# Kernel optimization log

Hardware: AMD Instinct MI355X
Metric: run time of the kernel (lower is better)

The kernel has to match this reference:

```python
import jax, jax.numpy as jnp
import numpy as np
from jax import lax

B, CHI, CHO, H, W = 8, 128, 128, 64, 64
K = 3
KK = K * K


def setup_inputs() -> dict:
    key = jax.random.key(0)
    ks = jax.random.split(key, 7)
    x = jax.random.normal(ks[0], (B, CHI, H, W), jnp.float32)
    # small offset-conv weights so sampled offsets stay in a realistic few-pixel range
    off_w = jax.random.normal(ks[1], (3 * KK, CHI, K, K), jnp.float32) * 0.01
    off_b = jnp.zeros((3 * KK,), jnp.float32)
    w = jax.random.normal(ks[2], (CHO, CHI, K, K), jnp.float32) / np.sqrt(CHI * KK).astype(np.float32)
    b = jnp.zeros((CHO,), jnp.float32)
    gamma = jax.random.uniform(ks[3], (CHO,), jnp.float32)  # nn.init.uniform_ on BN weight
    beta = jnp.zeros((CHO,), jnp.float32)
    return {"x": x, "off_w": off_w, "off_b": off_b, "w": w, "b": b, "gamma": gamma, "beta": beta}


def _deform_conv(x, off_w, off_b, w, b):
    """DCNv2 modulated deformable conv, k=3, stride=1, pad=1, dil=1, 1 deform group."""
    B_, C, H_, W_ = x.shape
    # offset/mask branch: plain 3x3 conv -> 27 channels (2*9 offsets, 9 masks)
    om = lax.conv_general_dilated(x, off_w, (1, 1), ((1, 1), (1, 1)),
                                  dimension_numbers=("NCHW", "OIHW", "NCHW"))
    om = om + off_b[None, :, None, None]
    off = om[:, : 2 * KK].reshape(B_, KK, 2, H_, W_)  # [B,9,2,H,W]; ch 2k=y, 2k+1=x
    mask = jax.nn.sigmoid(om[:, 2 * KK:])             # [B,9,H,W]

    ky, kx = jnp.meshgrid(jnp.arange(K, dtype=jnp.float32),
                          jnp.arange(K, dtype=jnp.float32), indexing="ij")
    ky = ky.reshape(KK); kx = kx.reshape(KK)
    # sampling positions: p = p0 - pad + k*dil + offset
    py = off[:, :, 0] + (jnp.arange(H_, dtype=jnp.float32) - 1.0)[None, None, :, None] + ky[None, :, None, None]
    px = off[:, :, 1] + (jnp.arange(W_, dtype=jnp.float32) - 1.0)[None, None, None, :] + kx[None, :, None, None]

    y0 = jnp.floor(py); x0 = jnp.floor(px)
    ly = py - y0; lx = px - x0
    xf = x.reshape(B_, C, H_ * W_)

    def corner(yi, xi, wgt):
        valid = ((yi >= 0) & (yi <= H_ - 1) & (xi >= 0) & (xi <= W_ - 1)).astype(x.dtype)
        yc = jnp.clip(yi, 0, H_ - 1).astype(jnp.int32)
        xc = jnp.clip(xi, 0, W_ - 1).astype(jnp.int32)
        idx = (yc * W_ + xc).reshape(B_, KK * H_ * W_)
        g = jax.vmap(lambda xb, ib: xb[:, ib])(xf, idx).reshape(B_, C, KK, H_, W_)
        return g * (valid * wgt)[:, None]

    val = (corner(y0, x0, (1 - ly) * (1 - lx))
           + corner(y0, x0 + 1, (1 - ly) * lx)
           + corner(y0 + 1, x0, ly * (1 - lx))
           + corner(y0 + 1, x0 + 1, ly * lx))  # [B,C,9,H,W]
    val = val * mask[:, None]  # modulation
    out = jnp.einsum("bckhw,ock->bohw", val, w.reshape(w.shape[0], C, KK))
    return out + b[None, :, None, None]


def reference(x, off_w, off_b, w, b, gamma, beta):
    y = _deform_conv(x, off_w, off_b, w, b)
    # BatchNorm2d in training mode (batch statistics), eps=1e-5, then ReLU
    mean = y.mean(axis=(0, 2, 3))
    var = y.var(axis=(0, 2, 3))
    yn = (y - mean[None, :, None, None]) * lax.rsqrt(var[None, :, None, None] + 1e-5)
    return jax.nn.relu(yn * gamma[None, :, None, None] + beta[None, :, None, None])
```

## Files before the change

kernel.cpp:

```cpp
#include <hip/hip_runtime.h>
#include <hip/hip_bf16.h>
#include <math.h>

#define HH 64
#define WW 64
#define HW 4096
#define LDV 136

typedef __bf16 bf16x8 __attribute__((ext_vector_type(8)));
typedef float floatx4 __attribute__((ext_vector_type(4)));
typedef unsigned int uint4a __attribute__((ext_vector_type(4)));
typedef unsigned int uint2a __attribute__((ext_vector_type(2)));

#define WS_Y    0u
#define WS_PSQ  16777216u
#define WS_XTB  16778240u
#define WS_WTB  25166848u
#define WS_OWB  25461760u

static __device__ inline ushort f2bf(float f) {
  __hip_bfloat16 h = __float2bfloat16(f);
  return __builtin_bit_cast(ushort, h);
}
static __device__ inline float lo16(unsigned int u) { return __builtin_bit_cast(float, u << 16); }
static __device__ inline float hi16(unsigned int u) { return __builtin_bit_cast(float, u & 0xffff0000u); }

__global__ __launch_bounds__(256) void k_prep(const float* __restrict__ x,
                                              const float* __restrict__ w,
                                              const float* __restrict__ ow,
                                              ushort* __restrict__ xtb,
                                              ushort* __restrict__ wtb,
                                              ushort* __restrict__ owb,
                                              float* __restrict__ psq) {
  __shared__ float tile[32][33];
  int bid = blockIdx.x;
  if (bid < 4096) {
    int hw0 = (bid & 127) * 32;
    int c0 = ((bid >> 7) & 3) * 32;
    int b = bid >> 9;
    int col = threadIdx.x & 31, row = threadIdx.x >> 5;
    const float* xb = x + ((size_t)b * 128 + c0) * HW + hw0;
#pragma unroll
    for (int i = 0; i < 32; i += 8)
      tile[row + i][col] = xb[(size_t)(row + i) * HW + col];
    __syncthreads();
    int hw = threadIdx.x >> 3, cq = threadIdx.x & 7;
    ushort* xo = xtb + ((size_t)b * HW + hw0) * 128 + c0;
    unsigned int lo = (unsigned int)f2bf(tile[cq * 4 + 0][hw]) |
                      ((unsigned int)f2bf(tile[cq * 4 + 1][hw]) << 16);
    unsigned int hi = (unsigned int)f2bf(tile[cq * 4 + 2][hw]) |
                      ((unsigned int)f2bf(tile[cq * 4 + 3][hw]) << 16);
    uint2a v2 = (uint2a){lo, hi};
    *(uint2a*)(&xo[(size_t)hw * 128 + cq * 4]) = v2;
  } else if (bid < 4096 + 576) {
    int idx = (bid - 4096) * 256 + threadIdx.x;
    int c = idx & 127, o = (idx >> 7) & 127, k = idx >> 14;
    wtb[idx] = f2bf(w[(o * 128 + c) * 9 + k]);
  } else if (bid < 4096 + 720) {
    int j = (bid - 4672) * 256 + threadIdx.x;
    int c = j & 127, o = (j >> 7) & 31, k = j >> 12;
    float v = (o < 27) ? ow[(o * 128 + c) * 9 + k] : 0.f;
    owb[j] = f2bf(v);
  } else {
    psq[threadIdx.x] = 0.f;
  }
}

__global__ __launch_bounds__(256) void k_main(
    const ushort* __restrict__ xtb, const ushort* __restrict__ wtb,
    const ushort* __restrict__ owb, const float* __restrict__ off_b,
    const float* __restrict__ bias, float* __restrict__ y) {
  __shared__ alignas(16) ushort Vl[2][32 * LDV];
  __shared__ float omL[27 * 32];
  int t = threadIdx.x;
  int lane = t & 63, wv = t >> 6;
  int li = lane & 15, quad = lane >> 4;
  int hr = blockIdx.x;
  int row = hr >> 1, p0b = (hr & 1) * 32;
  int b = blockIdx.y;
  const ushort* xb = xtb + (size_t)b * HW * 128;
  int ch = t & 15;
  int pq = t >> 4;

  int mi = wv & 1, ni = wv >> 1;
  floatx4 oacc = (floatx4){0.f, 0.f, 0.f, 0.f};
  uint4a u0, u1;
  auto p1load = [&](int k, int p, uint4a& u) {
    int ky = k / 3, kx = k % 3;
    int ry = row - 1 + ky, cx = p0b + p - 1 + kx;
    bool v = (ry >= 0 && ry < HH && cx >= 0 && cx < WW);
    int idx = v ? (ry * WW + cx) : 0;
    uint4a a = *(const uint4a*)(xb + (size_t)idx * 128 + ch * 8);
    u = v ? a : (uint4a){0u, 0u, 0u, 0u};
  };
  p1load(0, pq, u0);
  p1load(0, pq + 16, u1);
  for (int k = 0; k < 9; ++k) {
    *(uint4a*)(&Vl[k & 1][pq * LDV + ch * 8]) = u0;
    *(uint4a*)(&Vl[k & 1][(pq + 16) * LDV + ch * 8]) = u1;
    if (k < 8) {
      p1load(k + 1, pq, u0);
      p1load(k + 1, pq + 16, u1);
    }
    __syncthreads();
#pragma unroll
    for (int ks = 0; ks < 4; ++ks) {
      bf16x8 bfrag = __builtin_bit_cast(bf16x8,
          *(const uint4a*)(&Vl[k & 1][(ni * 16 + li) * LDV + ks * 32 + quad * 8]));
      bf16x8 afrag = __builtin_bit_cast(bf16x8,
          *(const uint4a*)(&owb[(size_t)(k * 32 + mi * 16 + li) * 128 + ks * 32 + quad * 8]));
      oacc = __builtin_amdgcn_mfma_f32_16x16x32_bf16(afrag, bfrag, oacc, 0, 0, 0);
    }
  }
#pragma unroll
  for (int r = 0; r < 4; ++r) {
    int o = mi * 16 + quad * 4 + r;
    if (o < 27) omL[o * 32 + ni * 16 + li] = oacc[r] + off_b[o];
  }
  __syncthreads();

  floatx4 macc[8][2];
#pragma unroll
  for (int g = 0; g < 8; ++g) {
    macc[g][0] = (floatx4){0.f, 0.f, 0.f, 0.f};
    macc[g][1] = (floatx4){0.f, 0.f, 0.f, 0.f};
  }

  float wqA[4], wqB[4];
  int idxA[4], idxB[4];
  uint4a u[8];

  auto prep = [&](int k, int p, float* wq, int* idx4) {
    int ky = k / 3, kx = k % 3;
    float offy = omL[(2 * k) * 32 + p];
    float offx = omL[(2 * k + 1) * 32 + p];
    float mraw = omL[(18 + k) * 32 + p];
    float m = 1.f / (1.f + __expf(-mraw));
    float py = offy + (float)(row - 1 + ky);
    float px = offx + (float)(p0b + p - 1 + kx);
    float y0f = floorf(py), x0f = floorf(px);
    float ly = py - y0f, lx = px - x0f;
    int iy0 = (int)y0f, ix0 = (int)x0f;
    int iy1 = iy0 + 1, ix1 = ix0 + 1;
    float w00 = (1.f - ly) * (1.f - lx) * m, w01 = (1.f - ly) * lx * m;
    float w10 = ly * (1.f - lx) * m, w11 = ly * lx * m;
    if (iy0 < 0 || iy0 > HH - 1) { w00 = 0.f; w01 = 0.f; }
    if (iy1 < 0 || iy1 > HH - 1) { w10 = 0.f; w11 = 0.f; }
    if (ix0 < 0 || ix0 > WW - 1) { w00 = 0.f; w10 = 0.f; }
    if (ix1 < 0 || ix1 > WW - 1) { w01 = 0.f; w11 = 0.f; }
    int cy0 = min(max(iy0, 0), HH - 1), cy1 = min(max(iy1, 0), HH - 1);
    int cx0 = min(max(ix0, 0), WW - 1), cx1 = min(max(ix1, 0), WW - 1);
    idx4[0] = cy0 * WW + cx0;
    idx4[1] = cy0 * WW + cx1;
    idx4[2] = cy1 * WW + cx0;
    idx4[3] = cy1 * WW + cx1;
    wq[0] = w00; wq[1] = w01; wq[2] = w10; wq[3] = w11;
  };
  auto issue = [&]() {
#pragma unroll
    for (int c = 0; c < 4; ++c)
      u[c] = *(const uint4a*)(xb + (size_t)idxA[c] * 128 + wv * 32 + quad * 8);
#pragma unroll
    for (int c = 0; c < 4; ++c)
      u[4 + c] = *(const uint4a*)(xb + (size_t)idxB[c] * 128 + wv * 32 + quad * 8);
  };

  prep(0, li, wqA, idxA);
  prep(0, 16 + li, wqB, idxB);
  issue();
  for (int k = 0; k < 9; ++k) {
    uint4a bv0, bv1;
#pragma unroll
    for (int e = 0; e < 4; ++e) {
      float rlo = wqA[0] * lo16(u[0][e]) + wqA[1] * lo16(u[1][e]) +
                  wqA[2] * lo16(u[2][e]) + wqA[3] * lo16(u[3][e]);
      float rhi = wqA[0] * hi16(u[0][e]) + wqA[1] * hi16(u[1][e]) +
                  wqA[2] * hi16(u[2][e]) + wqA[3] * hi16(u[3][e]);
      bv0[e] = (unsigned int)f2bf(rlo) | ((unsigned int)f2bf(rhi) << 16);
      float slo = wqB[0] * lo16(u[4][e]) + wqB[1] * lo16(u[5][e]) +
                  wqB[2] * lo16(u[6][e]) + wqB[3] * lo16(u[7][e]);
      float shi = wqB[0] * hi16(u[4][e]) + wqB[1] * hi16(u[5][e]) +
                  wqB[2] * hi16(u[6][e]) + wqB[3] * hi16(u[7][e]);
      bv1[e] = (unsigned int)f2bf(slo) | ((unsigned int)f2bf(shi) << 16);
    }
    bf16x8 b0 = __builtin_bit_cast(bf16x8, bv0);
    bf16x8 b1 = __builtin_bit_cast(bf16x8, bv1);
    if (k < 8) {
      prep(k + 1, li, wqA, idxA);
      prep(k + 1, 16 + li, wqB, idxB);
      issue();
    }
    const ushort* Arow = wtb + (size_t)k * 128 * 128 + wv * 32 + quad * 8;
#pragma unroll
    for (int g = 0; g < 8; ++g) {
      bf16x8 a = __builtin_bit_cast(bf16x8,
          *(const uint4a*)(Arow + (size_t)(g * 16 + li) * 128));
      macc[g][0] = __builtin_amdgcn_mfma_f32_16x16x32_bf16(a, b0, macc[g][0], 0, 0, 0);
      macc[g][1] = __builtin_amdgcn_mfma_f32_16x16x32_bf16(a, b1, macc[g][1], 0, 0, 0);
    }
  }

  float (*red)[8] = (float(*)[8])(&Vl[0][0]);
  for (int g = 0; g < 8; ++g) {
    int ow = g & 3;
    __syncthreads();
    if (wv != ow) {
      int slot = wv - (wv > ow ? 1 : 0);
#pragma unroll
      for (int pt = 0; pt < 2; ++pt)
#pragma unroll
        for (int r = 0; r < 4; ++r)
          red[slot * 64 + lane][pt * 4 + r] = macc[g][pt][r];
    }
    __syncthreads();
    if (wv == ow) {
#pragma unroll
      for (int slot = 0; slot < 3; ++slot)
#pragma unroll
        for (int pt = 0; pt < 2; ++pt)
#pragma unroll
          for (int r = 0; r < 4; ++r)
            macc[g][pt][r] += red[slot * 64 + lane][pt * 4 + r];
    }
  }
#pragma unroll
  for (int gg = 0; gg < 2; ++gg) {
    int g = wv + gg * 4;
#pragma unroll
    for (int pt = 0; pt < 2; ++pt)
#pragma unroll
      for (int r = 0; r < 4; ++r) {
        int o = g * 16 + quad * 4 + r;
        int p = p0b + pt * 16 + li;
        y[((size_t)(b * 128 + o)) * HW + row * 64 + p] = macc[g][pt][r] + bias[o];
      }
  }
}

__global__ __launch_bounds__(256) void k_stats(const float* __restrict__ y,
                                               float* __restrict__ psq) {
  int o = blockIdx.x, b = blockIdx.y, t = threadIdx.x;
  const float4* yb = (const float4*)(y + ((size_t)(b * 128 + o)) * HW);
  float s = 0.f, q = 0.f;
#pragma unroll
  for (int i = 0; i < 4; ++i) {
    float4 v = yb[t + i * 256];
    s += v.x + v.y + v.z + v.w;
    q += v.x * v.x + v.y * v.y + v.z * v.z + v.w * v.w;
  }
#pragma unroll
  for (int off = 32; off >= 1; off >>= 1) {
    s += __shfl_down(s, off, 64);
    q += __shfl_down(q, off, 64);
  }
  __shared__ float bs[4], bq[4];
  if ((t & 63) == 0) { bs[t >> 6] = s; bq[t >> 6] = q; }
  __syncthreads();
  if (t == 0) {
    atomicAdd(&psq[o], bs[0] + bs[1] + bs[2] + bs[3]);
    atomicAdd(&psq[128 + o], bq[0] + bq[1] + bq[2] + bq[3]);
  }
}

__global__ __launch_bounds__(256) void k_norm(const float* __restrict__ y,
                                              const float* __restrict__ psq,
                                              const float* __restrict__ gamma,
                                              const float* __restrict__ beta,
                                              float* __restrict__ out) {
  int blk = blockIdx.x;
  int o = (blk >> 2) & 127;
  float s = psq[o], q = psq[128 + o];
  float mean = s * (1.f / 32768.f);
  float var = q * (1.f / 32768.f) - mean * mean;
  float scale = gamma[o] * rsqrtf(var + 1e-5f);
  float shift = beta[o] - mean * scale;
  int i4 = blk * 256 + threadIdx.x;
  float4 v = ((const float4*)y)[i4];
  float4 r;
  r.x = fmaxf(v.x * scale + shift, 0.f);
  r.y = fmaxf(v.y * scale + shift, 0.f);
  r.z = fmaxf(v.z * scale + shift, 0.f);
  r.w = fmaxf(v.w * scale + shift, 0.f);
  ((float4*)out)[i4] = r;
}

extern "C" void kernel_launch(void* const* d_in, const int* in_sizes, int n_in,
                              void* d_out, int out_size, void* d_ws, size_t ws_size,
                              hipStream_t stream) {
  const float* x     = (const float*)d_in[0];
  const float* off_w = (const float*)d_in[1];
  const float* off_b = (const float*)d_in[2];
  const float* w     = (const float*)d_in[3];
  const float* bias  = (const float*)d_in[4];
  const float* gamma = (const float*)d_in[5];
  const float* beta  = (const float*)d_in[6];
  float* out = (float*)d_out;
  char* ws = (char*)d_ws;

  float* y    = (float*)(ws + WS_Y);
  float* psq  = (float*)(ws + WS_PSQ);
  ushort* xtb = (ushort*)(ws + WS_XTB);
  ushort* wtb = (ushort*)(ws + WS_WTB);
  ushort* owb = (ushort*)(ws + WS_OWB);

  k_prep<<<4817, 256, 0, stream>>>(x, w, off_w, xtb, wtb, owb, psq);
  k_main<<<dim3(128, 8), 256, 0, stream>>>(xtb, wtb, owb, off_b, bias, y);
  k_stats<<<dim3(128, 8), 256, 0, stream>>>(y, psq);
  k_norm<<<4096, 256, 0, stream>>>(y, psq, gamma, beta, out);
}
```

Baseline: 193.6 us.

## Repartition deform-conv waves by pixel half and channel half

Each wave now owns 16 pixels and half of the input channels, rather than all 32 pixels and a quarter of the channels. The offset-conv stage loads its operands straight from global memory into registers, so the LDS staging buffer and its per-tap barriers are gone. The final cross-wave reduction shrinks to a single two-way exchange through LDS, replacing eight rounds of four-way reduction with 16 barriers. Accumulator registers drop from 64 to 32 floats, and launch bounds of 4 are added to raise occupancy; the cost is more redundant weight loads per wave.

```diff
diff --git a/kernel.cpp b/kernel.cpp
--- a/kernel.cpp
+++ b/kernel.cpp
@@ -5,7 +5,6 @@
 #define HH 64
 #define WW 64
 #define HW 4096
-#define LDV 136
 
 typedef __bf16 bf16x8 __attribute__((ext_vector_type(8)));
 typedef float floatx4 __attribute__((ext_vector_type(4)));
@@ -66,78 +65,90 @@
   }
 }
 
-__global__ __launch_bounds__(256) void k_main(
+__global__ __launch_bounds__(256, 4) void k_main(
     const ushort* __restrict__ xtb, const ushort* __restrict__ wtb,
     const ushort* __restrict__ owb, const float* __restrict__ off_b,
     const float* __restrict__ bias, float* __restrict__ y) {
-  __shared__ alignas(16) ushort Vl[2][32 * LDV];
+  __shared__ alignas(16) float red[4224];
   __shared__ float omL[27 * 32];
   int t = threadIdx.x;
   int lane = t & 63, wv = t >> 6;
   int li = lane & 15, quad = lane >> 4;
+  int kh = wv >> 1, ph = wv & 1;
   int hr = blockIdx.x;
   int row = hr >> 1, p0b = (hr & 1) * 32;
   int b = blockIdx.y;
   const ushort* xb = xtb + (size_t)b * HW * 128;
-  int ch = t & 15;
-  int pq = t >> 4;
-
-  int mi = wv & 1, ni = wv >> 1;
-  floatx4 oacc = (floatx4){0.f, 0.f, 0.f, 0.f};
-  uint4a u0, u1;
-  auto p1load = [&](int k, int p, uint4a& u) {
+  int pix = 16 * ph + li;
+
+  const uint4a zero4 = (uint4a){0u, 0u, 0u, 0u};
+  floatx4 oaccP[2];
+  oaccP[0] = (floatx4){0.f, 0.f, 0.f, 0.f};
+  oaccP[1] = (floatx4){0.f, 0.f, 0.f, 0.f};
+  uint4a ub[2];
+  auto p1load = [&](int k) {
     int ky = k / 3, kx = k % 3;
-    int ry = row - 1 + ky, cx = p0b + p - 1 + kx;
+    int ry = row - 1 + ky, cx = p0b + pix - 1 + kx;
     bool v = (ry >= 0 && ry < HH && cx >= 0 && cx < WW);
     int idx = v ? (ry * WW + cx) : 0;
-    uint4a a = *(const uint4a*)(xb + (size_t)idx * 128 + ch * 8);
-    u = v ? a : (uint4a){0u, 0u, 0u, 0u};
+    const ushort* base = xb + (size_t)idx * 128 + kh * 64 + quad * 8;
+    uint4a a0 = *(const uint4a*)(base);
+    uint4a a1 = *(const uint4a*)(base + 32);
+    ub[0] = v ? a0 : zero4;
+    ub[1] = v ? a1 : zero4;
   };
-  p1load(0, pq, u0);
-  p1load(0, pq + 16, u1);
+  p1load(0);
   for (int k = 0; k < 9; ++k) {
-    *(uint4a*)(&Vl[k & 1][pq * LDV + ch * 8]) = u0;
-    *(uint4a*)(&Vl[k & 1][(pq + 16) * LDV + ch * 8]) = u1;
-    if (k < 8) {
-      p1load(k + 1, pq, u0);
-      p1load(k + 1, pq + 16, u1);
-    }
-    __syncthreads();
-#pragma unroll
-    for (int ks = 0; ks < 4; ++ks) {
-      bf16x8 bfrag = __builtin_bit_cast(bf16x8,
-          *(const uint4a*)(&Vl[k & 1][(ni * 16 + li) * LDV + ks * 32 + quad * 8]));
-      bf16x8 afrag = __builtin_bit_cast(bf16x8,
-          *(const uint4a*)(&owb[(size_t)(k * 32 + mi * 16 + li) * 128 + ks * 32 + quad * 8]));
-      oacc = __builtin_amdgcn_mfma_f32_16x16x32_bf16(afrag, bfrag, oacc, 0, 0, 0);
-    }
-  }
-#pragma unroll
-  for (int r = 0; r < 4; ++r) {
-    int o = mi * 16 + quad * 4 + r;
-    if (o < 27) omL[o * 32 + ni * 16 + li] = oacc[r] + off_b[o];
+    bf16x8 b0 = __builtin_bit_cast(bf16x8, ub[0]);
+    bf16x8 b1 = __builtin_bit_cast(bf16x8, ub[1]);
+    if (k < 8) p1load(k + 1);
+#pragma unroll
+    for (int g = 0; g < 2; ++g) {
+      const ushort* Ab = owb + (size_t)(k * 32 + g * 16 + li) * 128 + kh * 64 + quad * 8;
+      bf16x8 a0 = __builtin_bit_cast(bf16x8, *(const uint4a*)(Ab));
+      bf16x8 a1 = __builtin_bit_cast(bf16x8, *(const uint4a*)(Ab + 32));
+      oaccP[g] = __builtin_amdgcn_mfma_f32_16x16x32_bf16(a0, b0, oaccP[g], 0, 0, 0);
+      oaccP[g] = __builtin_amdgcn_mfma_f32_16x16x32_bf16(a1, b1, oaccP[g], 0, 0, 0);
+    }
+  }
+  if (kh == 1) {
+#pragma unroll
+    for (int g = 0; g < 2; ++g)
+#pragma unroll
+      for (int r = 0; r < 4; ++r)
+        red[(ph * 64 + lane) * 9 + g * 4 + r] = oaccP[g][r];
   }
   __syncthreads();
-
-  floatx4 macc[8][2];
-#pragma unroll
-  for (int g = 0; g < 8; ++g) {
-    macc[g][0] = (floatx4){0.f, 0.f, 0.f, 0.f};
-    macc[g][1] = (floatx4){0.f, 0.f, 0.f, 0.f};
-  }
-
-  float wqA[4], wqB[4];
-  int idxA[4], idxB[4];
+  if (kh == 0) {
+#pragma unroll
+    for (int g = 0; g < 2; ++g)
+#pragma unroll
+      for (int r = 0; r < 4; ++r) {
+        int o = g * 16 + quad * 4 + r;
+        if (o < 27) {
+          float v = oaccP[g][r] + red[(ph * 64 + lane) * 9 + g * 4 + r];
+          omL[o * 32 + pix] = v + off_b[o];
+        }
+      }
+  }
+  __syncthreads();
+
+  floatx4 macc[8];
+#pragma unroll
+  for (int g = 0; g < 8; ++g) macc[g] = (floatx4){0.f, 0.f, 0.f, 0.f};
+
+  float wq[4];
+  int idx4[4];
   uint4a u[8];
 
-  auto prep = [&](int k, int p, float* wq, int* idx4) {
+  auto prep = [&](int k) {
     int ky = k / 3, kx = k % 3;
-    float offy = omL[(2 * k) * 32 + p];
-    float offx = omL[(2 * k + 1) * 32 + p];
-    float mraw = omL[(18 + k) * 32 + p];
+    float offy = omL[(2 * k) * 32 + pix];
+    float offx = omL[(2 * k + 1) * 32 + pix];
+    float mraw = omL[(18 + k) * 32 + pix];
     float m = 1.f / (1.f + __expf(-mraw));
     float py = offy + (float)(row - 1 + ky);
-    float px = offx + (float)(p0b + p - 1 + kx);
+    float px = offx + (float)(p0b + pix - 1 + kx);
     float y0f = floorf(py), x0f = floorf(px);
     float ly = py - y0f, lx = px - x0f;
     int iy0 = (int)y0f, ix0 = (int)x0f;
@@ -158,81 +169,63 @@
   };
   auto issue = [&]() {
 #pragma unroll
-    for (int c = 0; c < 4; ++c)
-      u[c] = *(const uint4a*)(xb + (size_t)idxA[c] * 128 + wv * 32 + quad * 8);
-#pragma unroll
-    for (int c = 0; c < 4; ++c)
-      u[4 + c] = *(const uint4a*)(xb + (size_t)idxB[c] * 128 + wv * 32 + quad * 8);
+    for (int c = 0; c < 4; ++c) {
+      const ushort* base = xb + (size_t)idx4[c] * 128 + kh * 64 + quad * 8;
+      u[c * 2] = *(const uint4a*)(base);
+      u[c * 2 + 1] = *(const uint4a*)(base + 32);
+    }
   };
 
-  prep(0, li, wqA, idxA);
-  prep(0, 16 + li, wqB, idxB);
+  prep(0);
   issue();
   for (int k = 0; k < 9; ++k) {
     uint4a bv0, bv1;
 #pragma unroll
     for (int e = 0; e < 4; ++e) {
-      float rlo = wqA[0] * lo16(u[0][e]) + wqA[1] * lo16(u[1][e]) +
-                  wqA[2] * lo16(u[2][e]) + wqA[3] * lo16(u[3][e]);
-      float rhi = wqA[0] * hi16(u[0][e]) + wqA[1] * hi16(u[1][e]) +
-                  wqA[2] * hi16(u[2][e]) + wqA[3] * hi16(u[3][e]);
+      float rlo = wq[0] * lo16(u[0][e]) + wq[1] * lo16(u[2][e]) +
+                  wq[2] * lo16(u[4][e]) + wq[3] * lo16(u[6][e]);
+      float rhi = wq[0] * hi16(u[0][e]) + wq[1] * hi16(u[2][e]) +
+                  wq[2] * hi16(u[4][e]) + wq[3] * hi16(u[6][e]);
       bv0[e] = (unsigned int)f2bf(rlo) | ((unsigned int)f2bf(rhi) << 16);
-      float slo = wqB[0] * lo16(u[4][e]) + wqB[1] * lo16(u[5][e]) +
-                  wqB[2] * lo16(u[6][e]) + wqB[3] * lo16(u[7][e]);
-      float shi = wqB[0] * hi16(u[4][e]) + wqB[1] * hi16(u[5][e]) +
-                  wqB[2] * hi16(u[6][e]) + wqB[3] * hi16(u[7][e]);
+      float slo = wq[0] * lo16(u[1][e]) + wq[1] * lo16(u[3][e]) +
+                  wq[2] * lo16(u[5][e]) + wq[3] * lo16(u[7][e]);
+      float shi = wq[0] * hi16(u[1][e]) + wq[1] * hi16(u[3][e]) +
+                  wq[2] * hi16(u[5][e]) + wq[3] * hi16(u[7][e]);
       bv1[e] = (unsigned int)f2bf(slo) | ((unsigned int)f2bf(shi) << 16);
     }
     bf16x8 b0 = __builtin_bit_cast(bf16x8, bv0);
     bf16x8 b1 = __builtin_bit_cast(bf16x8, bv1);
     if (k < 8) {
-      prep(k + 1, li, wqA, idxA);
-      prep(k + 1, 16 + li, wqB, idxB);
+      prep(k + 1);
       issue();
     }
-    const ushort* Arow = wtb + (size_t)k * 128 * 128 + wv * 32 + quad * 8;
+    const ushort* Ak = wtb + (size_t)k * 128 * 128 + kh * 64 + quad * 8;
 #pragma unroll
     for (int g = 0; g < 8; ++g) {
-      bf16x8 a = __builtin_bit_cast(bf16x8,
-          *(const uint4a*)(Arow + (size_t)(g * 16 + li) * 128));
-      macc[g][0] = __builtin_amdgcn_mfma_f32_16x16x32_bf16(a, b0, macc[g][0], 0, 0, 0);
-      macc[g][1] = __builtin_amdgcn_mfma_f32_16x16x32_bf16(a, b1, macc[g][1], 0, 0, 0);
-    }
-  }
-
-  float (*red)[8] = (float(*)[8])(&Vl[0][0]);
-  for (int g = 0; g < 8; ++g) {
-    int ow = g & 3;
-    __syncthreads();
-    if (wv != ow) {
-      int slot = wv - (wv > ow ? 1 : 0);
-#pragma unroll
-      for (int pt = 0; pt < 2; ++pt)
-#pragma unroll
-        for (int r = 0; r < 4; ++r)
-          red[slot * 64 + lane][pt * 4 + r] = macc[g][pt][r];
-    }
-    __syncthreads();
-    if (wv == ow) {
-#pragma unroll
-      for (int slot = 0; slot < 3; ++slot)
-#pragma unroll
-        for (int pt = 0; pt < 2; ++pt)
-#pragma unroll
-          for (int r = 0; r < 4; ++r)
-            macc[g][pt][r] += red[slot * 64 + lane][pt * 4 + r];
-    }
-  }
-#pragma unroll
-  for (int gg = 0; gg < 2; ++gg) {
-    int g = wv + gg * 4;
-#pragma unroll
-    for (int pt = 0; pt < 2; ++pt)
+      const ushort* Ab = Ak + (size_t)(g * 16 + li) * 128;
+      bf16x8 a0 = __builtin_bit_cast(bf16x8, *(const uint4a*)(Ab));
+      bf16x8 a1 = __builtin_bit_cast(bf16x8, *(const uint4a*)(Ab + 32));
+      macc[g] = __builtin_amdgcn_mfma_f32_16x16x32_bf16(a0, b0, macc[g], 0, 0, 0);
+      macc[g] = __builtin_amdgcn_mfma_f32_16x16x32_bf16(a1, b1, macc[g], 0, 0, 0);
+    }
+  }
+
+  if (kh == 1) {
+#pragma unroll
+    for (int g = 0; g < 8; ++g)
+#pragma unroll
+      for (int r = 0; r < 4; ++r)
+        red[(ph * 64 + lane) * 33 + g * 4 + r] = macc[g][r];
+  }
+  __syncthreads();
+  if (kh == 0) {
+#pragma unroll
+    for (int g = 0; g < 8; ++g)
 #pragma unroll
       for (int r = 0; r < 4; ++r) {
         int o = g * 16 + quad * 4 + r;
-        int p = p0b + pt * 16 + li;
-        y[((size_t)(b * 128 + o)) * HW + row * 64 + p] = macc[g][pt][r] + bias[o];
+        float v = macc[g][r] + red[(ph * 64 + lane) * 33 + g * 4 + r] + bias[o];
+        y[((size_t)(b * 128 + o)) * HW + row * 64 + p0b + pix] = v;
       }
   }
 }
```

New measurement: 212.6 us. +9.8%, slower.
